# Kernel optimization log

Measured on AMD Instinct MI355X. Metric: run time of the kernel, lower is better.

## Reference

```python
import jax, jax.numpy as jnp
import numpy as np

N6 = 100000
N8 = 100000
E = 400000
D = 128


def setup_inputs() -> dict:
    key = jax.random.key(0)
    ks = jax.random.split(key, 12)
    def msg(k):
        return jax.random.normal(k, (E, D), dtype=jnp.float32)
    def W(k):
        return jax.random.normal(k, (D, D), dtype=jnp.float32) / np.sqrt(D)
    def ei(k, n):
        return jax.random.randint(k, (E, 2), 0, n, dtype=jnp.int32)
    return {
        "msg_66": msg(ks[0]), "msg_68": msg(ks[1]),
        "msg_86": msg(ks[2]), "msg_88": msg(ks[3]),
        "W_66": W(ks[4]), "W_68": W(ks[5]), "W_86": W(ks[6]), "W_88": W(ks[7]),
        "ei_66": ei(ks[8], N6), "ei_68": ei(ks[9], N8),
        "ei_86": ei(ks[10], N6), "ei_88": ei(ks[11], N8),
        "num_nodes_6": N6, "num_nodes_8": N8,
    }


def _scatter_mean(v, dst, num_nodes):
    # torch_scatter reduce='mean': sum / count, count clamped to >=1 (zeros stay zero)
    s = jax.ops.segment_sum(v, dst, num_segments=num_nodes)
    c = jax.ops.segment_sum(jnp.ones((dst.shape[0],), v.dtype), dst, num_segments=num_nodes)
    return s / jnp.maximum(c, 1.0)[:, None]


def _proj_scatter(msg, W, ei, num_nodes):
    # per-edge-type linear (bias=False) then scatter-mean to dst nodes
    out = _scatter_mean(msg @ W, ei[:, 1], num_nodes)          # (num_nodes, D)
    # non-zero-row indicator (computed on detached values in the original)
    mask = jnp.any(jax.lax.stop_gradient(out) != 0, axis=-1).astype(out.dtype)  # (num_nodes,)
    return out, mask


def reference(msg_66, msg_68, msg_86, msg_88,
              W_66, W_68, W_86, W_88,
              ei_66, ei_68, ei_86, ei_88,
              num_nodes_6, num_nodes_8):
    # dict iteration order: "6-6", "6-8", "8-6", "8-8"; dst type is last token of key
    o66, m66 = _proj_scatter(msg_66, W_66, ei_66, num_nodes_6)
    o68, m68 = _proj_scatter(msg_68, W_68, ei_68, num_nodes_8)
    o86, m86 = _proj_scatter(msg_86, W_86, ei_86, num_nodes_6)
    o88, m88 = _proj_scatter(msg_88, W_88, ei_88, num_nodes_8)
    out_6 = jnp.stack([o66, o86], axis=1)   # (N6, num_edge_types_to_6=2, D)
    out_8 = jnp.stack([o68, o88], axis=1)   # (N8, 2, D)
    num_types_6 = m66 + m86                 # (N6,)
    num_types_8 = m68 + m88                 # (N8,)
    return out_6, out_8, num_types_6, num_types_8
```

## Files before the change

kernel.cpp:

```cpp
#include <hip/hip_runtime.h>

#define DF    128
#define EPB   1024
#define MAXB  512
#define TPB   64
#define CAP   512

typedef __attribute__((ext_vector_type(8))) short short8;
typedef __attribute__((ext_vector_type(4))) float f32x4;

__device__ __forceinline__ unsigned short f2bf(float x) {
    unsigned u = __float_as_uint(x);
    u = (u + 0x7FFFu + ((u >> 16) & 1u)) >> 16;
    return (unsigned short)u;
}
__device__ __forceinline__ unsigned pack2bf(float a, float b) {
    return (unsigned)f2bf(a) | ((unsigned)f2bf(b) << 16);
}
__device__ __forceinline__ int rfl(int x) {
    return __builtin_amdgcn_readfirstlane(x);
}

struct AllParams {
    const float* msg[4];
    const float* Wm[4];
    float*       outp[4];
    int gb[4];
    int eb[4];
    int N[4];
    int cum[5];
};


__global__ void __launch_bounds__(256) count_kernel(
    const int* __restrict__ ei66, const int* __restrict__ ei86,
    const int* __restrict__ ei68, const int* __restrict__ ei88,
    int E66, int E86, int E68, int E88, int N6, int N8,
    int* __restrict__ base)
{
    int Etot = E66 + E86 + E68 + E88;
    for (int gid = blockIdx.x * 256 + threadIdx.x; gid < Etot;
         gid += gridDim.x * 256) {
        int le = gid, nb, dst;
        if (le < E66)               { dst = ei66[2 * le + 1]; nb = 0; }
        else if ((le -= E66) < E86) { dst = ei86[2 * le + 1]; nb = N6; }
        else if ((le -= E86) < E68) { dst = ei68[2 * le + 1]; nb = 2 * N6; }
        else { le -= E68;             dst = ei88[2 * le + 1]; nb = 2 * N6 + N8; }
        atomicAdd(base + nb + dst, 1);
    }
}

__global__ void __launch_bounds__(256) scan1_kernel(
    int* __restrict__ data, int M, int* __restrict__ bsum)
{
    __shared__ int ts[256];
    int t = threadIdx.x;
    int i0 = blockIdx.x * EPB + t * 4;
    int v0 = 0, v1 = 0, v2 = 0, v3 = 0;
    if (i0 + 3 < M) {
        int4 q = *(const int4*)(data + i0);
        v0 = q.x; v1 = q.y; v2 = q.z; v3 = q.w;
    } else {
        if (i0     < M) v0 = data[i0];
        if (i0 + 1 < M) v1 = data[i0 + 1];
        if (i0 + 2 < M) v2 = data[i0 + 2];
    }
    int sum = v0 + v1 + v2 + v3;
    ts[t] = sum;
    __syncthreads();
    for (int off = 1; off < 256; off <<= 1) {
        int x = (t >= off) ? ts[t - off] : 0;
        __syncthreads();
        ts[t] += x;
        __syncthreads();
    }
    int excl = ts[t] - sum;
    if (t == 255) bsum[blockIdx.x] = ts[255];
    int w0 = excl, w1 = excl + v0, w2 = w1 + v1, w3 = w2 + v2;
    if (i0 + 3 < M) {
        *(int4*)(data + i0) = make_int4(w0, w1, w2, w3);
    } else {
        if (i0     < M) data[i0]     = w0;
        if (i0 + 1 < M) data[i0 + 1] = w1;
        if (i0 + 2 < M) data[i0 + 2] = w2;
    }
}

__global__ void __launch_bounds__(256) scan2_kernel(int* __restrict__ bsum, int nb)
{
    __shared__ int s[MAXB];
    int t = threadIdx.x;
    s[t]       = (t       < nb) ? bsum[t]       : 0;
    s[t + 256] = (t + 256 < nb) ? bsum[t + 256] : 0;
    __syncthreads();
    int o0 = s[t], o1 = s[t + 256];
    for (int off = 1; off < MAXB; off <<= 1) {
        int a = (t       >= off) ? s[t       - off] : 0;
        int b = (t + 256 >= off) ? s[t + 256 - off] : 0;
        __syncthreads();
        s[t] += a; s[t + 256] += b;
        __syncthreads();
    }
    if (t       < nb) bsum[t]       = s[t]       - o0;
    if (t + 256 < nb) bsum[t + 256] = s[t + 256] - o1;
}

__global__ void __launch_bounds__(256) scan3_kernel(
    int* __restrict__ data, int M, const int* __restrict__ bsum)
{
    int add = bsum[blockIdx.x];
    if (add == 0) return;
    int i0 = blockIdx.x * EPB + threadIdx.x * 4;
    if (i0 + 3 < M) {
        int4 q = *(const int4*)(data + i0);
        q.x += add; q.y += add; q.z += add; q.w += add;
        *(int4*)(data + i0) = q;
    } else {
        if (i0     < M) data[i0]     += add;
        if (i0 + 1 < M) data[i0 + 1] += add;
        if (i0 + 2 < M) data[i0 + 2] += add;
    }
}

__global__ void __launch_bounds__(256) fill_kernel(
    const int* __restrict__ ei66, const int* __restrict__ ei86,
    const int* __restrict__ ei68, const int* __restrict__ ei88,
    int E66, int E86, int E68, int E88, int N6, int N8,
    int* __restrict__ base, int* __restrict__ csr)
{
    int Etot = E66 + E86 + E68 + E88;
    for (int gid = blockIdx.x * 256 + threadIdx.x; gid < Etot;
         gid += gridDim.x * 256) {
        int le = gid, nb, dst;
        if (le < E66)               { dst = ei66[2 * le + 1]; nb = 0; }
        else if ((le -= E66) < E86) { dst = ei86[2 * le + 1]; nb = N6; }
        else if ((le -= E86) < E68) { dst = ei68[2 * le + 1]; nb = 2 * N6; }
        else { le -= E68;             dst = ei88[2 * le + 1]; nb = 2 * N6 + N8; }
        int pos = atomicAdd(base + nb + dst, 1);
        csr[pos] = (int)((unsigned)gid | (((unsigned)(dst & 63)) << 26));
    }
}

__global__ void __launch_bounds__(256, 3) gather_mfma_kernel(
    const int* __restrict__ base, const int* __restrict__ csr, AllParams P)
{
    __shared__ alignas(16) short Wt[DF * DF];
    __shared__ alignas(16) short At[4][16 * DF];
    __shared__ int eids[CAP];
    __shared__ int ends_s[TPB + 1];

    const int t    = threadIdx.x;
    const int lane = t & 63;
    const int w    = t >> 6;
    const int l15  = lane & 15;
    const int lg   = lane >> 4;
    short* Atw = At[w];

    int curty = -1;
    const int T = P.cum[4];

    for (int tt = blockIdx.x * 2; tt < blockIdx.x * 2 + 2 && tt < T; ++tt) {
        const int ty = (tt >= P.cum[2]) ? ((tt >= P.cum[3]) ? 3 : 2)
                                        : ((tt >= P.cum[1]) ? 1 : 0);
        const float* msg = P.msg[ty];
        const int gbase = P.gb[ty], ebase = P.eb[ty], N = P.N[ty];
        const int n0 = (tt - P.cum[ty]) * TPB;

        __syncthreads();

        if (ty != curty) {
            const float* Wm = P.Wm[ty];
            for (int idx = t; idx < 2048; idx += 256) {
                int k0 = (idx >> 5) << 1;
                int ng = (idx & 31) << 2;
                float4 wa = *(const float4*)(Wm + (size_t)k0 * DF + ng);
                float4 wb = *(const float4*)(Wm + (size_t)(k0 + 1) * DF + ng);
                float wav[4] = {wa.x, wa.y, wa.z, wa.w};
                float wbv[4] = {wb.x, wb.y, wb.z, wb.w};
                int cb = k0 >> 3, kl = k0 & 7;
                #pragma unroll
                for (int j = 0; j < 4; ++j) {
                    int n = ng + j;
                    int chunk = cb ^ (n & 7);
                    *(unsigned*)(Wt + n * DF + chunk * 8 + kl) =
                        pack2bf(wav[j], wbv[j]);
                }
            }
            curty = ty;
        }

        if (t <= TPB) {
            int nn = n0 + t - 1;
            if (nn >= N) nn = N - 1;
            int gi = gbase + nn;
            ends_s[t] = (gi >= 0) ? base[gi] : 0;
        }
        {
            int gi0   = gbase + n0 - 1;
            int myts0 = (gi0 >= 0) ? base[gi0] : 0;
            int nn = n0 + TPB - 1; if (nn >= N) nn = N - 1;
            int myts1 = base[gbase + nn];
            int tot_all = myts1 - myts0;
            for (int i = t; i < tot_all && i < CAP; i += 256)
                eids[i] = csr[myts0 + i];
        }
        __syncthreads();

        const int ts0   = ends_s[0];
        const int wrow0 = w * 16;
        const int s0    = ends_s[wrow0];
        const int s1    = ends_s[wrow0 + 16];
        const int lbase = s0 - ts0;
        const int tot   = s1 - s0;
        int   cur = wrow0;
        float ax = 0.f, ay = 0.f;

#define LDE(eX, sb) { _Pragma("unroll")                                       \
        for (int j = 0; j < 8; ++j) {                                         \
            int ls = (sb) + j; ls = (ls < tot) ? ls : (tot - 1);              \
            int gs = lbase + ls;                                              \
            eX[j] = (gs < CAP) ? eids[gs] : csr[ts0 + gs]; } }

#define LDM(vX, eX) { _Pragma("unroll")                                       \
        for (int j = 0; j < 8; ++j) {                                         \
            int idx = (int)(((unsigned)eX[j]) & 0x03FFFFFFu) - ebase;         \
            vX[j] = *(const float2*)(msg + (size_t)idx * DF + 2 * lane); } }

#define FLUSHR() {                                                            \
        int lr_ = cur & 15;                                                   \
        *(unsigned*)(Atw + lr_ * DF + ((((lane >> 2) ^ (lr_ & 7))) << 3)      \
                     + ((lane & 3) << 1)) = pack2bf(ax, ay);                  \
        ax = 0.f; ay = 0.f; ++cur; }

#define CONSB(vX, eX, sb) { _Pragma("unroll")                                 \
        for (int j = 0; j < 8; ++j) {                                         \
            if ((sb) + j < tot) {                                             \
                int rl = wrow0 + (int)((((unsigned)rfl(eX[j])) >> 26) & 15u); \
                while (cur < rl) FLUSHR();                                    \
                ax += vX[j].x; ay += vX[j].y; } } }

        if (tot > 0) {
            int eA[8], eB[8], eC[8], eD[8];
            float2 vA[8], vB[8], vC[8], vD[8];
            const int nb = (tot + 7) >> 3;

            LDE(eA, 0); LDE(eB, 8); LDE(eC, 16);
            LDM(vA, eA); LDM(vB, eB); LDM(vC, eC);
            int ib = 0;
            while (true) {
                LDE(eD, ib * 8 + 24); LDM(vD, eD); CONSB(vA, eA, ib * 8);
                if (++ib >= nb) break;
                LDE(eA, ib * 8 + 24); LDM(vA, eA); CONSB(vB, eB, ib * 8);
                if (++ib >= nb) break;
                LDE(eB, ib * 8 + 24); LDM(vB, eB); CONSB(vC, eC, ib * 8);
                if (++ib >= nb) break;
                LDE(eC, ib * 8 + 24); LDM(vC, eC); CONSB(vD, eD, ib * 8);
                if (++ib >= nb) break;
            }
        }
        while (cur < wrow0 + 16) FLUSHR();
#undef LDE
#undef LDM
#undef FLUSHR
#undef CONSB

        f32x4 acc[8];
        #pragma unroll
        for (int j = 0; j < 8; ++j) acc[j] = (f32x4){0.f, 0.f, 0.f, 0.f};

        #pragma unroll
        for (int kk = 0; kk < 4; ++kk) {
            int c = kk * 4 + lg;
            short8 av = *(const short8*)(Atw + l15 * DF
                                         + ((c ^ (l15 & 7)) << 3));
            #pragma unroll
            for (int j = 0; j < 8; ++j) {
                int n = j * 16 + l15;
                short8 bv = *(const short8*)(Wt + n * DF + ((c ^ (n & 7)) << 3));
                acc[j] = __builtin_amdgcn_mfma_f32_16x16x32_bf16(
                    av, bv, acc[j], 0, 0, 0);
            }
        }

        #pragma unroll
        for (int q = 0; q < 4; ++q) {
            int lrow = wrow0 + lg * 4 + q;
            int dg = ends_s[lrow + 1] - ends_s[lrow];
            float inv = (dg > 0) ? (1.0f / (float)dg) : 0.0f;
            #pragma unroll
            for (int j = 0; j < 8; ++j) acc[j][q] *= inv;
        }

        float* fA = (float*)Atw;
        float* outp = P.outp[ty];
        #pragma unroll
        for (int h = 0; h < 2; ++h) {
            if ((lg >> 1) == h) {
                int lr = (lg & 1) << 2;
                #pragma unroll
                for (int q = 0; q < 4; ++q)
                    #pragma unroll
                    for (int j = 0; j < 8; ++j)
                        fA[(lr + q) * DF + j * 16 + l15] = acc[j][q];
            }
            asm volatile("" ::: "memory");
            #pragma unroll
            for (int rr = 0; rr < 4; ++rr) {
                int lrh  = 2 * rr + (lane >> 5);
                int node = n0 + wrow0 + 8 * h + lrh;
                float4 x = *(const float4*)(fA + lrh * DF + (lane & 31) * 4);
                if (node < N)
                    *(float4*)(outp + (size_t)node * 256 + (lane & 31) * 4) = x;
            }
            asm volatile("" ::: "memory");
        }
    }
}

__global__ void __launch_bounds__(256) mask_kernel(
    const int* __restrict__ base, float* __restrict__ nt6,
    float* __restrict__ nt8, int N6, int N8)
{
    int i = blockIdx.x * blockDim.x + threadIdx.x;
    if (i < N6) {
        int g66 = i, g86 = N6 + i;
        int d66 = base[g66] - (g66 ? base[g66 - 1] : 0);
        int d86 = base[g86] - base[g86 - 1];
        nt6[i] = (float)((d66 > 0) + (d86 > 0));
    }
    if (i < N8) {
        int g68 = 2 * N6 + i, g88 = 2 * N6 + N8 + i;
        int d68 = base[g68] - base[g68 - 1];
        int d88 = base[g88] - base[g88 - 1];
        nt8[i] = (float)((d68 > 0) + (d88 > 0));
    }
}

extern "C" void kernel_launch(void* const* d_in, const int* in_sizes, int n_in,
                              void* d_out, int out_size, void* d_ws, size_t ws_size,
                              hipStream_t stream)
{
    const float* msg66 = (const float*)d_in[0];
    const float* msg68 = (const float*)d_in[1];
    const float* msg86 = (const float*)d_in[2];
    const float* msg88 = (const float*)d_in[3];
    const float* W66   = (const float*)d_in[4];
    const float* W68   = (const float*)d_in[5];
    const float* W86   = (const float*)d_in[6];
    const float* W88   = (const float*)d_in[7];
    const int*   ei66  = (const int*)d_in[8];
    const int*   ei68  = (const int*)d_in[9];
    const int*   ei86  = (const int*)d_in[10];
    const int*   ei88  = (const int*)d_in[11];

    int E66 = in_sizes[8]  / 2;
    int E68 = in_sizes[9]  / 2;
    int E86 = in_sizes[10] / 2;
    int E88 = in_sizes[11] / 2;
    int Etot = E66 + E86 + E68 + E88;

    size_t S  = (size_t)out_size / 257;
    int    N6 = (int)(S / 2);
    int    N8 = (int)(S - S / 2);
    int    M  = 2 * N6 + 2 * N8;

    float* out  = (float*)d_out;
    float* out6 = out;
    float* out8 = out + (size_t)N6 * 256;
    float* nt6  = out + (size_t)(N6 + N8) * 256;
    float* nt8  = nt6 + N6;

    int* base = (int*)d_ws;
    int* bsum = base + M;
    int* csr  = bsum + MAXB;

    int NB = (M + EPB - 1) / EPB;

    hipMemsetAsync(base, 0, (size_t)M * sizeof(int), stream);

    int eg = (Etot + 255) / 256;
    if (eg > 4096) eg = 4096;
    count_kernel<<<dim3(eg), dim3(256), 0, stream>>>(
        ei66, ei86, ei68, ei88, E66, E86, E68, E88, N6, N8, base);

    scan1_kernel<<<dim3(NB), dim3(256), 0, stream>>>(base, M, bsum);
    scan2_kernel<<<dim3(1),  dim3(256), 0, stream>>>(bsum, NB);
    scan3_kernel<<<dim3(NB), dim3(256), 0, stream>>>(base, M, bsum);

    fill_kernel<<<dim3(eg), dim3(256), 0, stream>>>(
        ei66, ei86, ei68, ei88, E66, E86, E68, E88, N6, N8, base, csr);

    int t6 = (N6 + TPB - 1) / TPB, t8 = (N8 + TPB - 1) / TPB;
    AllParams P;
    P.msg[0] = msg66; P.Wm[0] = W66; P.outp[0] = out6;       P.gb[0] = 0;           P.eb[0] = 0;                P.N[0] = N6;
    P.msg[1] = msg86; P.Wm[1] = W86; P.outp[1] = out6 + 128; P.gb[1] = N6;          P.eb[1] = E66;              P.N[1] = N6;
    P.msg[2] = msg68; P.Wm[2] = W68; P.outp[2] = out8;       P.gb[2] = 2 * N6;      P.eb[2] = E66 + E86;        P.N[2] = N8;
    P.msg[3] = msg88; P.Wm[3] = W88; P.outp[3] = out8 + 128; P.gb[3] = 2 * N6 + N8; P.eb[3] = E66 + E86 + E68;  P.N[3] = N8;
    P.cum[0] = 0;
    P.cum[1] = t6;
    P.cum[2] = 2 * t6;
    P.cum[3] = 2 * t6 + t8;
    P.cum[4] = 2 * t6 + 2 * t8;

    int G = (P.cum[4] + 1) / 2;
    gather_mfma_kernel<<<dim3(G), dim3(256), 0, stream>>>(base, csr, P);

    int Nmax = (N6 > N8) ? N6 : N8;
    mask_kernel<<<dim3((Nmax + 255) / 256), dim3(256), 0, stream>>>(
        base, nt6, nt8, N6, N8);
}
```

Before: 458.7 us.

## Process two node tiles concurrently per 512-thread block sharing one weight tile

Each block now runs with 512 threads, and each half of the block handles one 64-node tile at the same time. Previously a 256-thread block processed its two tiles one after another. The bf16 weight matrix is loaded into shared memory once per block and shared by both halves, and all blocks of a block are assigned to a single edge type. The goal is more in-flight gather memory traffic per CU and no serial second iteration. The cost is more shared memory and registers per block, which may limit occupancy; the launch bounds now ask for 4 blocks per CU.

Result: faster. 442.6 us (-3.5%).

```diff
diff --git a/kernel.cpp b/kernel.cpp
--- a/kernel.cpp
+++ b/kernel.cpp
@@ -28,7 +28,8 @@
     int gb[4];
     int eb[4];
     int N[4];
-    int cum[5];
+    int tcnt[4];
+    int cumB[5];
 };
 
 
@@ -141,179 +142,180 @@
     }
 }
 
-__global__ void __launch_bounds__(256, 3) gather_mfma_kernel(
+__global__ void __launch_bounds__(512, 4) gather_mfma_kernel(
     const int* __restrict__ base, const int* __restrict__ csr, AllParams P)
 {
     __shared__ alignas(16) short Wt[DF * DF];
-    __shared__ alignas(16) short At[4][16 * DF];
-    __shared__ int eids[CAP];
-    __shared__ int ends_s[TPB + 1];
+    __shared__ alignas(16) short At[8][16 * DF];
+    __shared__ int eids[2][CAP];
+    __shared__ int ends_s[2][TPB + 1];
 
     const int t    = threadIdx.x;
     const int lane = t & 63;
     const int w    = t >> 6;
+    const int hf   = w >> 2;
+    const int wl   = w & 3;
+    const int tl   = t & 255;
     const int l15  = lane & 15;
     const int lg   = lane >> 4;
     short* Atw = At[w];
 
-    int curty = -1;
-    const int T = P.cum[4];
-
-    for (int tt = blockIdx.x * 2; tt < blockIdx.x * 2 + 2 && tt < T; ++tt) {
-        const int ty = (tt >= P.cum[2]) ? ((tt >= P.cum[3]) ? 3 : 2)
-                                        : ((tt >= P.cum[1]) ? 1 : 0);
-        const float* msg = P.msg[ty];
-        const int gbase = P.gb[ty], ebase = P.eb[ty], N = P.N[ty];
-        const int n0 = (tt - P.cum[ty]) * TPB;
-
-        __syncthreads();
-
-        if (ty != curty) {
-            const float* Wm = P.Wm[ty];
-            for (int idx = t; idx < 2048; idx += 256) {
-                int k0 = (idx >> 5) << 1;
-                int ng = (idx & 31) << 2;
-                float4 wa = *(const float4*)(Wm + (size_t)k0 * DF + ng);
-                float4 wb = *(const float4*)(Wm + (size_t)(k0 + 1) * DF + ng);
-                float wav[4] = {wa.x, wa.y, wa.z, wa.w};
-                float wbv[4] = {wb.x, wb.y, wb.z, wb.w};
-                int cb = k0 >> 3, kl = k0 & 7;
-                #pragma unroll
-                for (int j = 0; j < 4; ++j) {
-                    int n = ng + j;
-                    int chunk = cb ^ (n & 7);
-                    *(unsigned*)(Wt + n * DF + chunk * 8 + kl) =
-                        pack2bf(wav[j], wbv[j]);
-                }
+    const int bb = blockIdx.x;
+    const int ty = (bb >= P.cumB[2]) ? ((bb >= P.cumB[3]) ? 3 : 2)
+                                     : ((bb >= P.cumB[1]) ? 1 : 0);
+    const float* msg = P.msg[ty];
+    const int gbase = P.gb[ty], ebase = P.eb[ty], N = P.N[ty];
+    const int tile  = (bb - P.cumB[ty]) * 2 + hf;
+    const bool act  = (tile < P.tcnt[ty]);
+    const int n0    = tile * TPB;
+
+    {
+        const float* Wm = P.Wm[ty];
+        for (int idx = t; idx < 2048; idx += 512) {
+            int k0 = (idx >> 5) << 1;
+            int ng = (idx & 31) << 2;
+            float4 wa = *(const float4*)(Wm + (size_t)k0 * DF + ng);
+            float4 wb = *(const float4*)(Wm + (size_t)(k0 + 1) * DF + ng);
+            float wav[4] = {wa.x, wa.y, wa.z, wa.w};
+            float wbv[4] = {wb.x, wb.y, wb.z, wb.w};
+            int cb = k0 >> 3, kl = k0 & 7;
+            #pragma unroll
+            for (int j = 0; j < 4; ++j) {
+                int n = ng + j;
+                int chunk = cb ^ (n & 7);
+                *(unsigned*)(Wt + n * DF + chunk * 8 + kl) =
+                    pack2bf(wav[j], wbv[j]);
             }
-            curty = ty;
-        }
-
-        if (t <= TPB) {
-            int nn = n0 + t - 1;
+        }
+    }
+
+    if (tl <= TPB) {
+        int v = 0;
+        if (act) {
+            int nn = n0 + tl - 1;
             if (nn >= N) nn = N - 1;
             int gi = gbase + nn;
-            ends_s[t] = (gi >= 0) ? base[gi] : 0;
-        }
-        {
-            int gi0   = gbase + n0 - 1;
-            int myts0 = (gi0 >= 0) ? base[gi0] : 0;
-            int nn = n0 + TPB - 1; if (nn >= N) nn = N - 1;
-            int myts1 = base[gbase + nn];
-            int tot_all = myts1 - myts0;
-            for (int i = t; i < tot_all && i < CAP; i += 256)
-                eids[i] = csr[myts0 + i];
-        }
-        __syncthreads();
-
-        const int ts0   = ends_s[0];
-        const int wrow0 = w * 16;
-        const int s0    = ends_s[wrow0];
-        const int s1    = ends_s[wrow0 + 16];
-        const int lbase = s0 - ts0;
-        const int tot   = s1 - s0;
-        int   cur = wrow0;
-        float ax = 0.f, ay = 0.f;
+            v = (gi >= 0) ? base[gi] : 0;
+        }
+        ends_s[hf][tl] = v;
+    }
+    if (act) {
+        int gi0   = gbase + n0 - 1;
+        int myts0 = (gi0 >= 0) ? base[gi0] : 0;
+        int nn = n0 + TPB - 1; if (nn >= N) nn = N - 1;
+        int myts1 = base[gbase + nn];
+        int tot_all = myts1 - myts0;
+        for (int i = tl; i < tot_all && i < CAP; i += 256)
+            eids[hf][i] = csr[myts0 + i];
+    }
+    __syncthreads();
+
+    const int ts0   = ends_s[hf][0];
+    const int wrow0 = wl * 16;
+    const int s0    = ends_s[hf][wrow0];
+    const int s1    = ends_s[hf][wrow0 + 16];
+    const int lbase = s0 - ts0;
+    const int tot   = s1 - s0;
+    int   cur = wrow0;
+    float ax = 0.f, ay = 0.f;
 
 #define LDE(eX, sb) { _Pragma("unroll")                                       \
-        for (int j = 0; j < 8; ++j) {                                         \
-            int ls = (sb) + j; ls = (ls < tot) ? ls : (tot - 1);              \
-            int gs = lbase + ls;                                              \
-            eX[j] = (gs < CAP) ? eids[gs] : csr[ts0 + gs]; } }
+    for (int j = 0; j < 8; ++j) {                                             \
+        int ls = (sb) + j; ls = (ls < tot) ? ls : (tot - 1);                  \
+        int gs = lbase + ls;                                                  \
+        eX[j] = (gs < CAP) ? eids[hf][gs] : csr[ts0 + gs]; } }
 
 #define LDM(vX, eX) { _Pragma("unroll")                                       \
-        for (int j = 0; j < 8; ++j) {                                         \
-            int idx = (int)(((unsigned)eX[j]) & 0x03FFFFFFu) - ebase;         \
-            vX[j] = *(const float2*)(msg + (size_t)idx * DF + 2 * lane); } }
+    for (int j = 0; j < 8; ++j) {                                             \
+        int idx = (int)(((unsigned)eX[j]) & 0x03FFFFFFu) - ebase;             \
+        vX[j] = *(const float2*)(msg + (size_t)idx * DF + 2 * lane); } }
 
 #define FLUSHR() {                                                            \
-        int lr_ = cur & 15;                                                   \
-        *(unsigned*)(Atw + lr_ * DF + ((((lane >> 2) ^ (lr_ & 7))) << 3)      \
-                     + ((lane & 3) << 1)) = pack2bf(ax, ay);                  \
-        ax = 0.f; ay = 0.f; ++cur; }
+    int lr_ = cur & 15;                                                       \
+    *(unsigned*)(Atw + lr_ * DF + ((((lane >> 2) ^ (lr_ & 7))) << 3)          \
+                 + ((lane & 3) << 1)) = pack2bf(ax, ay);                      \
+    ax = 0.f; ay = 0.f; ++cur; }
 
 #define CONSB(vX, eX, sb) { _Pragma("unroll")                                 \
-        for (int j = 0; j < 8; ++j) {                                         \
-            if ((sb) + j < tot) {                                             \
-                int rl = wrow0 + (int)((((unsigned)rfl(eX[j])) >> 26) & 15u); \
-                while (cur < rl) FLUSHR();                                    \
-                ax += vX[j].x; ay += vX[j].y; } } }
-
-        if (tot > 0) {
-            int eA[8], eB[8], eC[8], eD[8];
-            float2 vA[8], vB[8], vC[8], vD[8];
-            const int nb = (tot + 7) >> 3;
-
-            LDE(eA, 0); LDE(eB, 8); LDE(eC, 16);
-            LDM(vA, eA); LDM(vB, eB); LDM(vC, eC);
-            int ib = 0;
-            while (true) {
-                LDE(eD, ib * 8 + 24); LDM(vD, eD); CONSB(vA, eA, ib * 8);
-                if (++ib >= nb) break;
-                LDE(eA, ib * 8 + 24); LDM(vA, eA); CONSB(vB, eB, ib * 8);
-                if (++ib >= nb) break;
-                LDE(eB, ib * 8 + 24); LDM(vB, eB); CONSB(vC, eC, ib * 8);
-                if (++ib >= nb) break;
-                LDE(eC, ib * 8 + 24); LDM(vC, eC); CONSB(vD, eD, ib * 8);
-                if (++ib >= nb) break;
-            }
-        }
-        while (cur < wrow0 + 16) FLUSHR();
+    for (int j = 0; j < 8; ++j) {                                             \
+        if ((sb) + j < tot) {                                                 \
+            int rl = wrow0 + (int)((((unsigned)rfl(eX[j])) >> 26) & 15u);     \
+            while (cur < rl) FLUSHR();                                        \
+            ax += vX[j].x; ay += vX[j].y; } } }
+
+    if (tot > 0) {
+        int eA[8], eB[8], eC[8], eD[8];
+        float2 vA[8], vB[8], vC[8], vD[8];
+        const int nb = (tot + 7) >> 3;
+
+        LDE(eA, 0); LDE(eB, 8); LDE(eC, 16);
+        LDM(vA, eA); LDM(vB, eB); LDM(vC, eC);
+        int ib = 0;
+        while (true) {
+            LDE(eD, ib * 8 + 24); LDM(vD, eD); CONSB(vA, eA, ib * 8);
+            if (++ib >= nb) break;
+            LDE(eA, ib * 8 + 24); LDM(vA, eA); CONSB(vB, eB, ib * 8);
+            if (++ib >= nb) break;
+            LDE(eB, ib * 8 + 24); LDM(vB, eB); CONSB(vC, eC, ib * 8);
+            if (++ib >= nb) break;
+            LDE(eC, ib * 8 + 24); LDM(vC, eC); CONSB(vD, eD, ib * 8);
+            if (++ib >= nb) break;
+        }
+    }
+    while (cur < wrow0 + 16) FLUSHR();
 #undef LDE
 #undef LDM
 #undef FLUSHR
 #undef CONSB
 
-        f32x4 acc[8];
+    f32x4 acc[8];
+    #pragma unroll
+    for (int j = 0; j < 8; ++j) acc[j] = (f32x4){0.f, 0.f, 0.f, 0.f};
+
+    #pragma unroll
+    for (int kk = 0; kk < 4; ++kk) {
+        int c = kk * 4 + lg;
+        short8 av = *(const short8*)(Atw + l15 * DF + ((c ^ (l15 & 7)) << 3));
         #pragma unroll
-        for (int j = 0; j < 8; ++j) acc[j] = (f32x4){0.f, 0.f, 0.f, 0.f};
-
+        for (int j = 0; j < 8; ++j) {
+            int n = j * 16 + l15;
+            short8 bv = *(const short8*)(Wt + n * DF + ((c ^ (n & 7)) << 3));
+            acc[j] = __builtin_amdgcn_mfma_f32_16x16x32_bf16(
+                av, bv, acc[j], 0, 0, 0);
+        }
+    }
+
+    #pragma unroll
+    for (int q = 0; q < 4; ++q) {
+        int lrow = wrow0 + lg * 4 + q;
+        int dg = ends_s[hf][lrow + 1] - ends_s[hf][lrow];
+        float inv = (dg > 0) ? (1.0f / (float)dg) : 0.0f;
         #pragma unroll
-        for (int kk = 0; kk < 4; ++kk) {
-            int c = kk * 4 + lg;
-            short8 av = *(const short8*)(Atw + l15 * DF
-                                         + ((c ^ (l15 & 7)) << 3));
+        for (int j = 0; j < 8; ++j) acc[j][q] *= inv;
+    }
+
+    float* fA = (float*)Atw;
+    float* outp = P.outp[ty];
+    #pragma unroll
+    for (int h = 0; h < 2; ++h) {
+        if ((lg >> 1) == h) {
+            int lr = (lg & 1) << 2;
             #pragma unroll
-            for (int j = 0; j < 8; ++j) {
-                int n = j * 16 + l15;
-                short8 bv = *(const short8*)(Wt + n * DF + ((c ^ (n & 7)) << 3));
-                acc[j] = __builtin_amdgcn_mfma_f32_16x16x32_bf16(
-                    av, bv, acc[j], 0, 0, 0);
-            }
-        }
-
+            for (int q = 0; q < 4; ++q)
+                #pragma unroll
+                for (int j = 0; j < 8; ++j)
+                    fA[(lr + q) * DF + j * 16 + l15] = acc[j][q];
+        }
+        asm volatile("" ::: "memory");
         #pragma unroll
-        for (int q = 0; q < 4; ++q) {
-            int lrow = wrow0 + lg * 4 + q;
-            int dg = ends_s[lrow + 1] - ends_s[lrow];
-            float inv = (dg > 0) ? (1.0f / (float)dg) : 0.0f;
-            #pragma unroll
-            for (int j = 0; j < 8; ++j) acc[j][q] *= inv;
-        }
-
-        float* fA = (float*)Atw;
-        float* outp = P.outp[ty];
-        #pragma unroll
-        for (int h = 0; h < 2; ++h) {
-            if ((lg >> 1) == h) {
-                int lr = (lg & 1) << 2;
-                #pragma unroll
-                for (int q = 0; q < 4; ++q)
-                    #pragma unroll
-                    for (int j = 0; j < 8; ++j)
-                        fA[(lr + q) * DF + j * 16 + l15] = acc[j][q];
-            }
-            asm volatile("" ::: "memory");
-            #pragma unroll
-            for (int rr = 0; rr < 4; ++rr) {
-                int lrh  = 2 * rr + (lane >> 5);
-                int node = n0 + wrow0 + 8 * h + lrh;
-                float4 x = *(const float4*)(fA + lrh * DF + (lane & 31) * 4);
-                if (node < N)
-                    *(float4*)(outp + (size_t)node * 256 + (lane & 31) * 4) = x;
-            }
-            asm volatile("" ::: "memory");
-        }
+        for (int rr = 0; rr < 4; ++rr) {
+            int lrh  = 2 * rr + (lane >> 5);
+            int node = n0 + wrow0 + 8 * h + lrh;
+            float4 x = *(const float4*)(fA + lrh * DF + (lane & 31) * 4);
+            if (act && node < N)
+                *(float4*)(outp + (size_t)node * 256 + (lane & 31) * 4) = x;
+        }
+        asm volatile("" ::: "memory");
     }
 }
 
@@ -391,19 +393,19 @@
         ei66, ei86, ei68, ei88, E66, E86, E68, E88, N6, N8, base, csr);
 
     int t6 = (N6 + TPB - 1) / TPB, t8 = (N8 + TPB - 1) / TPB;
+    int b6 = (t6 + 1) / 2,        b8 = (t8 + 1) / 2;
     AllParams P;
-    P.msg[0] = msg66; P.Wm[0] = W66; P.outp[0] = out6;       P.gb[0] = 0;           P.eb[0] = 0;                P.N[0] = N6;
-    P.msg[1] = msg86; P.Wm[1] = W86; P.outp[1] = out6 + 128; P.gb[1] = N6;          P.eb[1] = E66;              P.N[1] = N6;
-    P.msg[2] = msg68; P.Wm[2] = W68; P.outp[2] = out8;       P.gb[2] = 2 * N6;      P.eb[2] = E66 + E86;        P.N[2] = N8;
-    P.msg[3] = msg88; P.Wm[3] = W88; P.outp[3] = out8 + 128; P.gb[3] = 2 * N6 + N8; P.eb[3] = E66 + E86 + E68;  P.N[3] = N8;
-    P.cum[0] = 0;
-    P.cum[1] = t6;
-    P.cum[2] = 2 * t6;
-    P.cum[3] = 2 * t6 + t8;
-    P.cum[4] = 2 * t6 + 2 * t8;
-
-    int G = (P.cum[4] + 1) / 2;
-    gather_mfma_kernel<<<dim3(G), dim3(256), 0, stream>>>(base, csr, P);
+    P.msg[0] = msg66; P.Wm[0] = W66; P.outp[0] = out6;       P.gb[0] = 0;           P.eb[0] = 0;                P.N[0] = N6; P.tcnt[0] = t6;
+    P.msg[1] = msg86; P.Wm[1] = W86; P.outp[1] = out6 + 128; P.gb[1] = N6;          P.eb[1] = E66;              P.N[1] = N6; P.tcnt[1] = t6;
+    P.msg[2] = msg68; P.Wm[2] = W68; P.outp[2] = out8;       P.gb[2] = 2 * N6;      P.eb[2] = E66 + E86;        P.N[2] = N8; P.tcnt[2] = t8;
+    P.msg[3] = msg88; P.Wm[3] = W88; P.outp[3] = out8 + 128; P.gb[3] = 2 * N6 + N8; P.eb[3] = E66 + E86 + E68;  P.N[3] = N8; P.tcnt[3] = t8;
+    P.cumB[0] = 0;
+    P.cumB[1] = b6;
+    P.cumB[2] = 2 * b6;
+    P.cumB[3] = 2 * b6 + b8;
+    P.cumB[4] = 2 * b6 + 2 * b8;
+
+    gather_mfma_kernel<<<dim3(P.cumB[4]), dim3(512), 0, stream>>>(base, csr, P);
 
     int Nmax = (N6 > N8) ? N6 : N8;
     mask_kernel<<<dim3((Nmax + 255) / 256), dim3(256), 0, stream>>>(
```
